# Kernel tuning notes

Hardware: AMD Instinct MI355X
Metric: run time of the kernel (lower is better)

## Reference

```python
import jax, jax.numpy as jnp
import numpy as np

PATCH = 9  # local correlation window (must match init_kwargs)
B, C, H, W = 16, 512, 64, 64


def setup_inputs() -> dict:
    key = jax.random.key(0)
    k1, k2 = jax.random.split(key)
    feature1 = jax.random.normal(k1, (B, C, H, W), dtype=jnp.float32)
    feature2 = jax.random.normal(k2, (B, C, H, W), dtype=jnp.float32)
    return {"feature1": feature1, "feature2": feature2}


def _l2normalize(x):
    # matches torch: x / sqrt(sum(x^2, dim=1) + 1e-6)
    eps = 1e-6
    return x / jnp.sqrt(jnp.sum(x * x, axis=1, keepdims=True) + eps)


def reference(feature1, feature2):
    patch = PATCH
    max_d = patch // 2
    f1 = _l2normalize(feature1)
    f2 = _l2normalize(feature2)
    b, c, h, w = f1.shape
    # The torch code computes a full (hw x hw) corr volume then extracts
    # windowed diagonals with zero padding at borders. Equivalent direct form:
    # out[b, dh*patch+dw, y*w+x] = relu(<f2[:, y+dh-max_d, x+dw-max_d], f1[:, y, x]>)
    # with out-of-range f2 positions contributing exactly 0 (zero padding).
    f2p = jnp.pad(f2, ((0, 0), (0, 0), (max_d, max_d), (max_d, max_d)))
    # fixed small loop over patch^2 displacements (81), vectorized over b,c,h,w
    slices = [
        jnp.einsum('bchw,bchw->bhw', f2p[:, :, dh:dh + h, dw:dw + w], f1)
        for dh in range(patch) for dw in range(patch)
    ]
    corr = jnp.stack(slices, axis=1)            # (b, patch*patch, h, w)
    corr = corr.reshape(b, patch * patch, h * w)
    return jax.nn.relu(corr)
```

## Files before the change

kernel.cpp:

```cpp
#include <hip/hip_runtime.h>
#include <hip/hip_bf16.h>
#include <stdint.h>
#include <math.h>

#define NB 16
#define NC 512
#define NH 64
#define NW 64
#define HW 4096
#define TILE_H 8
#define TILE_W 16
#define HALO_H 16
#define HALO_W 24
#define NHALO (HALO_H * HALO_W)
#define A_ROWS (TILE_H * TILE_W)
#define KC 32
#define NCH (NC / KC)
#define ROWB 80
#define A_BASE 0
#define B_BASE (A_ROWS * ROWB)
#define S_BASE (B_BASE + NHALO * ROWB)
#define LDS_BYTES (S_BASE + 512 * 4)

using f32x4  = __attribute__((ext_vector_type(4))) float;
using bf16x8 = __attribute__((ext_vector_type(8))) short;
using i32x4  = __attribute__((ext_vector_type(4))) int;

__device__ __forceinline__ unsigned bf16r(float x) {
  unsigned u = __float_as_uint(x);
  u += 0x7fffu + ((u >> 16) & 1u);
  return u >> 16;
}

__global__ __launch_bounds__(512, 4)
void corr_mfma(const float* __restrict__ f1, const float* __restrict__ f2,
               float* __restrict__ out)
{
  alignas(16) __shared__ unsigned char smem[LDS_BYTES];
  float* snorm = reinterpret_cast<float*>(smem + S_BASE);

  const int tid = threadIdx.x;

  const int blk  = blockIdx.x;
  const int xcd  = blk & 7;
  const int slot = blk >> 3;
  const int b    = xcd * 2 + (slot >> 5);
  const int t5   = slot & 31;
  const int y0   = (t5 >> 2) * TILE_H;
  const int x0   = (t5 & 3) * TILE_W;

  const int lane = tid & 63;
  const int lr   = lane & 15;
  const int lk   = lane >> 4;
  const int wv   = tid >> 6;

  const float* gptr;
  uint32_t     lbase;
  bool         ok;
  {
    const int s = tid;
    if (s < A_ROWS) {
      const int ty = s >> 4, tx = s & 15;
      gptr  = f1 + (size_t)b * NC * HW + (size_t)(y0 + ty) * NW + (x0 + tx);
      lbase = A_BASE + (uint32_t)s * ROWB;
      ok    = true;
    } else {
      const int h  = s - A_ROWS;
      const int hy = h / HALO_W, hx = h % HALO_W;
      const int yy = y0 - 4 + hy, xx = x0 - 4 + hx;
      const bool v = ((unsigned)yy < NH) && ((unsigned)xx < NW);
      const size_t off = v ? ((size_t)b * NC * HW + (size_t)yy * NW + xx) : (size_t)0;
      gptr  = f2 + off;
      lbase = B_BASE + (uint32_t)h * ROWB;
      ok    = v;
    }
  }

  f32x4 acc[9][2];
  #pragma unroll
  for (int j = 0; j < 9; ++j)
    #pragma unroll
    for (int k = 0; k < 2; ++k) {
      f32x4 z = {0.f, 0.f, 0.f, 0.f};
      acc[j][k] = z;
    }

  float ss = 0.f;

  for (int kc = 0; kc < NCH; ++kc) {
    {
      const float* gp = gptr + (size_t)kc * KC * HW;
      float v[KC];
      if (ok) {
        #pragma unroll
        for (int k = 0; k < KC; ++k) v[k] = gp[(size_t)k * HW];
      } else {
        #pragma unroll
        for (int k = 0; k < KC; ++k) v[k] = 0.f;
      }
      float ps = 0.f;
      #pragma unroll
      for (int k = 0; k < KC; ++k) ps = fmaf(v[k], v[k], ps);
      ss += ps;

      unsigned char* lp = smem + lbase;
      #pragma unroll
      for (int j = 0; j < 4; ++j) {
        i32x4 w;
        #pragma unroll
        for (int q = 0; q < 4; ++q) {
          const unsigned lo = bf16r(v[j * 8 + 2 * q]);
          const unsigned hi = bf16r(v[j * 8 + 2 * q + 1]);
          w[q] = (int)((hi << 16) | lo);
        }
        *reinterpret_cast<i32x4*>(lp + j * 16) = w;
      }
    }
    __syncthreads();

    const bf16x8 afr = *reinterpret_cast<const bf16x8*>(
        smem + A_BASE + (uint32_t)(wv * 16 + lr) * ROWB + lk * 16);
    #pragma unroll
    for (int dh = 0; dh < 9; ++dh) {
      const int hy = wv + dh;
      #pragma unroll
      for (int hx0 = 0; hx0 < 2; ++hx0) {
        const bf16x8 bfr = *reinterpret_cast<const bf16x8*>(
            smem + B_BASE + (uint32_t)(hy * HALO_W + hx0 * 8 + lr) * ROWB + lk * 16);
        acc[dh][hx0] =
            __builtin_amdgcn_mfma_f32_16x16x32_bf16(afr, bfr, acc[dh][hx0], 0, 0, 0);
      }
    }
    __syncthreads();
  }

  snorm[tid] = ss;
  __syncthreads();
  {
    const float t = snorm[tid];
    snorm[tid] = 1.0f / sqrtf(t + 1e-6f);
  }
  __syncthreads();

  float* op = out + (size_t)b * 81 * HW;
  #pragma unroll
  for (int dh = 0; dh < 9; ++dh) {
    const int hy = wv + dh;
    #pragma unroll
    for (int hx0 = 0; hx0 < 2; ++hx0) {
      const f32x4 a4 = acc[dh][hx0];
      const float i2 = snorm[A_ROWS + hy * HALO_W + hx0 * 8 + lr];
      #pragma unroll
      for (int r = 0; r < 4; ++r) {
        const int m  = lk * 4 + r;
        const int dw = hx0 * 8 + lr - m;
        if (dw >= 0 && dw < 9) {
          const float i1 = snorm[wv * 16 + m];
          float val = a4[r] * i1 * i2;
          val = fmaxf(val, 0.f);
          op[(size_t)(dh * 9 + dw) * HW + (size_t)(y0 + wv) * NW + (x0 + m)] = val;
        }
      }
    }
  }
}

extern "C" void kernel_launch(void* const* d_in, const int* in_sizes, int n_in,
                              void* d_out, int out_size, void* d_ws, size_t ws_size,
                              hipStream_t stream) {
  (void)in_sizes; (void)n_in; (void)out_size; (void)d_ws; (void)ws_size;
  const float* f1 = (const float*)d_in[0];
  const float* f2 = (const float*)d_in[1];
  float* out = (float*)d_out;
  corr_mfma<<<dim3(512), dim3(512), 0, stream>>>(f1, f2, out);
}
```

Baseline: 316.1 us.

## Double-buffer LDS tiles and prefetch next channel chunk during MFMA compute

Splits LDS into two buffers so the global loads of the next 32-channel chunk are issued before the MFMA work on the current chunk, and the bf16 store goes into the other buffer. This cuts the per-chunk barrier count from two to one and aims to hide global load latency behind compute. The cost is twice the LDS footprint, and launch bounds drop to 2 blocks per CU, which may reduce occupancy.

After: 315.1 us. No clear change (-0.3%).

```diff
diff --git a/kernel.cpp b/kernel.cpp
--- a/kernel.cpp
+++ b/kernel.cpp
@@ -14,13 +14,14 @@
 #define HALO_W 24
 #define NHALO (HALO_H * HALO_W)
 #define A_ROWS (TILE_H * TILE_W)
+#define NROWS (A_ROWS + NHALO)
 #define KC 32
 #define NCH (NC / KC)
 #define ROWB 80
-#define A_BASE 0
-#define B_BASE (A_ROWS * ROWB)
-#define S_BASE (B_BASE + NHALO * ROWB)
-#define LDS_BYTES (S_BASE + 512 * 4)
+#define BUF0 0u
+#define BUF1 (NROWS * ROWB)
+#define SN_BASE (2u * NROWS * ROWB)
+#define LDS_BYTES (SN_BASE + NROWS * 4)
 
 using f32x4  = __attribute__((ext_vector_type(4))) float;
 using bf16x8 = __attribute__((ext_vector_type(8))) short;
@@ -32,12 +33,12 @@
   return u >> 16;
 }
 
-__global__ __launch_bounds__(512, 4)
+__global__ __launch_bounds__(512, 2)
 void corr_mfma(const float* __restrict__ f1, const float* __restrict__ f2,
                float* __restrict__ out)
 {
   alignas(16) __shared__ unsigned char smem[LDS_BYTES];
-  float* snorm = reinterpret_cast<float*>(smem + S_BASE);
+  float* snorm = reinterpret_cast<float*>(smem + SN_BASE);
 
   const int tid = threadIdx.x;
 
@@ -55,24 +56,24 @@
   const int wv   = tid >> 6;
 
   const float* gptr;
-  uint32_t     lbase;
+  uint32_t     rowoff;
   bool         ok;
   {
     const int s = tid;
     if (s < A_ROWS) {
       const int ty = s >> 4, tx = s & 15;
-      gptr  = f1 + (size_t)b * NC * HW + (size_t)(y0 + ty) * NW + (x0 + tx);
-      lbase = A_BASE + (uint32_t)s * ROWB;
-      ok    = true;
+      gptr   = f1 + (size_t)b * NC * HW + (size_t)(y0 + ty) * NW + (x0 + tx);
+      rowoff = (uint32_t)s * ROWB;
+      ok     = true;
     } else {
       const int h  = s - A_ROWS;
       const int hy = h / HALO_W, hx = h % HALO_W;
       const int yy = y0 - 4 + hy, xx = x0 - 4 + hx;
       const bool v = ((unsigned)yy < NH) && ((unsigned)xx < NW);
       const size_t off = v ? ((size_t)b * NC * HW + (size_t)yy * NW + xx) : (size_t)0;
-      gptr  = f2 + off;
-      lbase = B_BASE + (uint32_t)h * ROWB;
-      ok    = v;
+      gptr   = f2 + off;
+      rowoff = (uint32_t)s * ROWB;
+      ok     = v;
     }
   }
 
@@ -86,53 +87,72 @@
     }
 
   float ss = 0.f;
+  float v[KC];
 
-  for (int kc = 0; kc < NCH; ++kc) {
-    {
-      const float* gp = gptr + (size_t)kc * KC * HW;
-      float v[KC];
-      if (ok) {
-        #pragma unroll
-        for (int k = 0; k < KC; ++k) v[k] = gp[(size_t)k * HW];
-      } else {
-        #pragma unroll
-        for (int k = 0; k < KC; ++k) v[k] = 0.f;
+  auto load_chunk = [&](int kc) {
+    const float* gp = gptr + (size_t)kc * KC * HW;
+    if (ok) {
+      #pragma unroll
+      for (int k = 0; k < KC; ++k) v[k] = gp[(size_t)k * HW];
+    } else {
+      #pragma unroll
+      for (int k = 0; k < KC; ++k) v[k] = 0.f;
+    }
+  };
+
+  auto store_chunk = [&](uint32_t base) {
+    float ps = 0.f;
+    #pragma unroll
+    for (int k = 0; k < KC; ++k) ps = fmaf(v[k], v[k], ps);
+    ss += ps;
+    unsigned char* lp = smem + base + rowoff;
+    #pragma unroll
+    for (int j = 0; j < 4; ++j) {
+      i32x4 w;
+      #pragma unroll
+      for (int q = 0; q < 4; ++q) {
+        const unsigned lo = bf16r(v[j * 8 + 2 * q]);
+        const unsigned hi = bf16r(v[j * 8 + 2 * q + 1]);
+        w[q] = (int)((hi << 16) | lo);
       }
-      float ps = 0.f;
-      #pragma unroll
-      for (int k = 0; k < KC; ++k) ps = fmaf(v[k], v[k], ps);
-      ss += ps;
+      *reinterpret_cast<i32x4*>(lp + j * 16) = w;
+    }
+  };
 
-      unsigned char* lp = smem + lbase;
-      #pragma unroll
-      for (int j = 0; j < 4; ++j) {
-        i32x4 w;
-        #pragma unroll
-        for (int q = 0; q < 4; ++q) {
-          const unsigned lo = bf16r(v[j * 8 + 2 * q]);
-          const unsigned hi = bf16r(v[j * 8 + 2 * q + 1]);
-          w[q] = (int)((hi << 16) | lo);
-        }
-        *reinterpret_cast<i32x4*>(lp + j * 16) = w;
-      }
-    }
-    __syncthreads();
-
+  auto compute_chunk = [&](uint32_t base) {
     const bf16x8 afr = *reinterpret_cast<const bf16x8*>(
-        smem + A_BASE + (uint32_t)(wv * 16 + lr) * ROWB + lk * 16);
+        smem + base + (uint32_t)(wv * 16 + lr) * ROWB + lk * 16);
     #pragma unroll
     for (int dh = 0; dh < 9; ++dh) {
       const int hy = wv + dh;
       #pragma unroll
       for (int hx0 = 0; hx0 < 2; ++hx0) {
         const bf16x8 bfr = *reinterpret_cast<const bf16x8*>(
-            smem + B_BASE + (uint32_t)(hy * HALO_W + hx0 * 8 + lr) * ROWB + lk * 16);
+            smem + base + (uint32_t)(A_ROWS + hy * HALO_W + hx0 * 8 + lr) * ROWB + lk * 16);
         acc[dh][hx0] =
             __builtin_amdgcn_mfma_f32_16x16x32_bf16(afr, bfr, acc[dh][hx0], 0, 0, 0);
       }
     }
+  };
+
+  load_chunk(0);
+  store_chunk(BUF0);
+  __syncthreads();
+
+  #define PIPE_ITER(KCC, CUR, NXT)  \
+    load_chunk((KCC) + 1);          \
+    compute_chunk(CUR);             \
+    store_chunk(NXT);               \
     __syncthreads();
+
+  for (int k2 = 0; k2 < 7; ++k2) {
+    const int kc = 2 * k2;
+    PIPE_ITER(kc,     BUF0, BUF1)
+    PIPE_ITER(kc + 1, BUF1, BUF0)
   }
+  PIPE_ITER(14, BUF0, BUF1)
+  compute_chunk(BUF1);
+  #undef PIPE_ITER
 
   snorm[tid] = ss;
   __syncthreads();
```
